# Performance work log

Measured on AMD Instinct MI355X. Metric: run time of the kernel, lower is better.

The kernel has to match this reference:

```python
import jax, jax.numpy as jnp
import numpy as np

B, H, W, C = 32, 56, 56, 128
WS, NH, DEPTH = 7, 4, 2
SHIFT = WS // 2
N = WS * WS
HID = 4 * C
CPB = 512


def _layernorm(x, g, b, eps=1e-5):
    m = x.mean(-1, keepdims=True)
    v = ((x - m) ** 2).mean(-1, keepdims=True)
    return (x - m) * jax.lax.rsqrt(v + eps) * g + b


def _window_partition(x):
    b, h, w, c = x.shape
    x = x.reshape(b, h // WS, WS, w // WS, WS, c)
    return x.transpose(0, 1, 3, 2, 4, 5).reshape(-1, N, c)


def _window_reverse(xw, h, w):
    c = xw.shape[-1]
    b = xw.shape[0] // ((h // WS) * (w // WS))
    x = xw.reshape(b, h // WS, w // WS, WS, WS, c)
    return x.transpose(0, 1, 3, 2, 4, 5).reshape(b, h, w, c)


def _rel_index():
    coords = np.stack(np.meshgrid(np.arange(WS), np.arange(WS), indexing='ij'))
    flat = coords.reshape(2, -1)
    rel = (flat[:, :, None] - flat[:, None, :]).transpose(1, 2, 0).astype(np.int64)
    rel[..., 0] += WS - 1
    rel[..., 1] += WS - 1
    rel[..., 0] *= 2 * WS - 1
    return jnp.asarray(rel.sum(-1))  # [N, N]


def _coords_table():
    # SwinV2 log-spaced continuous relative coords table (pretrained_window_size=0 path)
    r = np.arange(-(WS - 1), WS, dtype=np.float32)
    t = np.stack(np.meshgrid(r, r, indexing='ij'), axis=-1)  # [2W-1, 2W-1, 2]
    t = t / (WS - 1) * 8.0
    t = np.sign(t) * np.log2(np.abs(t) + 1.0) / np.log2(8.0)
    return jnp.asarray(t.reshape(-1, 2))  # [(2W-1)^2, 2]


def _shift_mask():
    img = np.zeros((H, W), np.float32)
    cnt = 0
    for hs in (slice(0, -WS), slice(-WS, -SHIFT), slice(-SHIFT, None)):
        for ws_ in (slice(0, -WS), slice(-WS, -SHIFT), slice(-SHIFT, None)):
            img[hs, ws_] = cnt
            cnt += 1
    mw = np.asarray(_window_partition(jnp.asarray(img)[None, :, :, None])).reshape(-1, N)
    diff = mw[:, None, :] - mw[:, :, None]
    return jnp.asarray(np.where(diff != 0, -100.0, 0.0).astype(np.float32))  # [nW, N, N]


def _forward(x, qkv_w, q_bias, v_bias, logit_scale, cpb_w1, cpb_b1, cpb_w2,
             proj_w, proj_b, norm1_g, norm1_b, mlp_w1, mlp_b1, mlp_w2, mlp_b2,
             norm2_g, norm2_b, pm_g, pm_b, pm_w):
    rel_idx = _rel_index()
    table = _coords_table()
    smask = _shift_mask()
    for i in range(DEPTH):
        shift = 0 if i % 2 == 0 else SHIFT
        xs = jnp.roll(x, (-shift, -shift), axis=(1, 2)) if shift else x
        xw = _window_partition(xs)  # [B*nW, N, C]
        bias = jnp.concatenate([q_bias[i], jnp.zeros_like(q_bias[i]), v_bias[i]])
        qkv = (xw @ qkv_w[i] + bias).reshape(-1, N, 3, NH, C // NH).transpose(2, 0, 3, 1, 4)
        q, k, v = qkv[0], qkv[1], qkv[2]  # [B*nW, NH, N, hd]
        qn = q / jnp.maximum(jnp.linalg.norm(q, axis=-1, keepdims=True), 1e-12)
        kn = k / jnp.maximum(jnp.linalg.norm(k, axis=-1, keepdims=True), 1e-12)
        scale = jnp.exp(jnp.minimum(logit_scale[i], jnp.log(100.0)))  # [NH,1,1]
        attn = jnp.einsum('bhnd,bhmd->bhnm', qn, kn) * scale
        rpb = 16.0 * jax.nn.sigmoid(
            (jax.nn.relu(table @ cpb_w1[i] + cpb_b1[i]) @ cpb_w2[i])[rel_idx])  # [N,N,NH]
        attn = attn + rpb.transpose(2, 0, 1)[None]
        if shift:
            nW = smask.shape[0]
            attn = (attn.reshape(-1, nW, NH, N, N) + smask[None, :, None]).reshape(-1, NH, N, N)
        attn = jax.nn.softmax(attn, axis=-1)
        out = jnp.einsum('bhnm,bhmd->bnhd', attn, v).reshape(-1, N, C)
        out = out @ proj_w[i] + proj_b[i]
        xs = _window_reverse(out, H, W)
        if shift:
            xs = jnp.roll(xs, (shift, shift), axis=(1, 2))
        # SwinV2 post-norm residuals
        x = x + _layernorm(xs, norm1_g[i], norm1_b[i])
        y = jax.nn.gelu(x @ mlp_w1[i] + mlp_b1[i], approximate=False) @ mlp_w2[i] + mlp_b2[i]
        x = x + _layernorm(y, norm2_g[i], norm2_b[i])
    # PatchMerging: [B,H,W,C] -> [B,H/2,W/2,4C] -> norm -> Linear(4C,2C)
    xm = x.reshape(B, H // 2, 2, W // 2, 2, C).transpose(0, 1, 3, 2, 4, 5)
    xm = xm.reshape(B, H // 2, W // 2, 4 * C)
    return _layernorm(xm, pm_g, pm_b) @ pm_w


def setup_inputs() -> dict:
    key = jax.random.key(0)
    ks = jax.random.split(key, 8)
    s = 0.02
    rn = lambda k, shp: jax.random.normal(k, shp, jnp.float32) * s
    return dict(
        x=jax.random.normal(ks[0], (B, H, W, C), jnp.float32),
        qkv_w=rn(ks[1], (DEPTH, C, 3 * C)),
        q_bias=jnp.zeros((DEPTH, C), jnp.float32),
        v_bias=jnp.zeros((DEPTH, C), jnp.float32),
        logit_scale=jnp.full((DEPTH, NH, 1, 1), np.log(10.0), jnp.float32),
        cpb_w1=rn(ks[2], (DEPTH, 2, CPB)),
        cpb_b1=jnp.zeros((DEPTH, CPB), jnp.float32),
        cpb_w2=rn(ks[3], (DEPTH, CPB, NH)),
        proj_w=rn(ks[4], (DEPTH, C, C)),
        proj_b=jnp.zeros((DEPTH, C), jnp.float32),
        norm1_g=jnp.ones((DEPTH, C), jnp.float32),
        norm1_b=jnp.zeros((DEPTH, C), jnp.float32),
        mlp_w1=rn(ks[5], (DEPTH, C, HID)),
        mlp_b1=jnp.zeros((DEPTH, HID), jnp.float32),
        mlp_w2=rn(ks[6], (DEPTH, HID, C)),
        mlp_b2=jnp.zeros((DEPTH, C), jnp.float32),
        norm2_g=jnp.ones((DEPTH, C), jnp.float32),
        norm2_b=jnp.zeros((DEPTH, C), jnp.float32),
        pm_g=jnp.ones((4 * C,), jnp.float32),
        pm_b=jnp.zeros((4 * C,), jnp.float32),
        pm_w=rn(ks[7], (4 * C, 2 * C)),
    )


def reference(x, qkv_w, q_bias, v_bias, logit_scale, cpb_w1, cpb_b1, cpb_w2,
              proj_w, proj_b, norm1_g, norm1_b, mlp_w1, mlp_b1, mlp_w2, mlp_b2,
              norm2_g, norm2_b, pm_g, pm_b, pm_w):
    return _forward(x, qkv_w, q_bias, v_bias, logit_scale, cpb_w1, cpb_b1, cpb_w2,
                    proj_w, proj_b, norm1_g, norm1_b, mlp_w1, mlp_b1, mlp_w2, mlp_b2,
                    norm2_g, norm2_b, pm_g, pm_b, pm_w)
```

## Files before the change

kernel.cpp:

```cpp
#include <hip/hip_runtime.h>
#include <math.h>


namespace {
constexpr int kTok = 32 * 56 * 56;
}

typedef __attribute__((ext_vector_type(8))) short bf16x8;
typedef __attribute__((ext_vector_type(4))) float f32x4;

union FragU {
    int4 i4;
    bf16x8 b8;
    unsigned short u[8];
};

__device__ __forceinline__ short f2bf(float f) {
    unsigned u = __float_as_uint(f);
    return (short)((u + 0x7FFFu + ((u >> 16) & 1u)) >> 16);
}
__device__ __forceinline__ float bf2f(unsigned short u) {
    return __uint_as_float(((unsigned)u) << 16);
}
__device__ __forceinline__ unsigned cvt_pk_bf16(float a, float b) {
    unsigned r;
    asm("v_cvt_pk_bf16_f32 %0, %1, %2" : "=v"(r) : "v"(a), "v"(b));
    return r;
}
__device__ __forceinline__ float gelu_t(float x) {
    float x2 = x * x;
    float t0 = fmaf(0.044715f * x2, x, x);
    float e = exp2f(2.3022227f * t0);
    float r = __builtin_amdgcn_rcpf(e + 1.0f);
    return fmaf(-x, r, x);
}

__global__ __launch_bounds__(256) void k_cpb(
    const float* __restrict__ w1, const float* __restrict__ b1,
    const float* __restrict__ w2, float* __restrict__ out169) {
    int L = blockIdx.x / 169;
    int t = blockIdx.x % 169;
    const float* w1L = w1 + L * 1024;
    const float* b1L = b1 + L * 512;
    const float* w2L = w2 + L * 2048;
    float* outL = out169 + L * 704;
    int ia = t / 13, ib = t % 13;
    float r0 = (float)(ia - 6) * (8.0f / 6.0f);
    float s0 = (r0 > 0.f) ? 1.f : (r0 < 0.f ? -1.f : 0.f);
    float t0 = s0 * log2f(fabsf(r0) + 1.0f) * (1.0f / 3.0f);
    float r1 = (float)(ib - 6) * (8.0f / 6.0f);
    float s1 = (r1 > 0.f) ? 1.f : (r1 < 0.f ? -1.f : 0.f);
    float t1 = s1 * log2f(fabsf(r1) + 1.0f) * (1.0f / 3.0f);

    int tid = threadIdx.x;
    float p0 = 0, p1 = 0, p2 = 0, p3 = 0;
    for (int c = tid; c < 512; c += 256) {
        float hv = fmaxf(t0 * w1L[c] + t1 * w1L[512 + c] + b1L[c], 0.0f);
        p0 += hv * w2L[c * 4 + 0];
        p1 += hv * w2L[c * 4 + 1];
        p2 += hv * w2L[c * 4 + 2];
        p3 += hv * w2L[c * 4 + 3];
    }
    __shared__ float red[256][4];
    red[tid][0] = p0; red[tid][1] = p1; red[tid][2] = p2; red[tid][3] = p3;
    __syncthreads();
    for (int s = 128; s > 0; s >>= 1) {
        if (tid < s) {
            red[tid][0] += red[tid + s][0];
            red[tid][1] += red[tid + s][1];
            red[tid][2] += red[tid + s][2];
            red[tid][3] += red[tid + s][3];
        }
        __syncthreads();
    }
    if (tid < 4) outL[t * 4 + tid] = red[0][tid];
}

__global__ void k_rpb(const float* __restrict__ out169, float* __restrict__ rpb64) {
    int e2 = blockIdx.x * 256 + threadIdx.x;
    int L = e2 >> 14, e = e2 & 16383;
    int h = e >> 12, r = e & 4095;
    int i = r >> 6, j = r & 63;
    float val;
    if (j >= 49) {
        val = -30000.0f;
    } else if (i >= 49) {
        val = 0.0f;
    } else {
        int dp = i / 7 - j / 7 + 6;
        int dq = i % 7 - j % 7 + 6;
        float v = out169[L * 704 + (dp * 13 + dq) * 4 + h];
        val = 16.0f / (1.0f + expf(-v));
    }
    rpb64[e2] = val;
}

__device__ __forceinline__ void cvt_slot(
    const float* __restrict__ W, short* __restrict__ Wb, int slt, int Kb, int N) {
    int nn = slt & 63;
    int tmp = slt >> 6;
    int kb = tmp % Kb;
    int nt = tmp / Kb;
    int n = nt * 64 + nn;
    int k0 = kb * 8;
    union { int4 i4; short s8[8]; } u;
#pragma unroll
    for (int e = 0; e < 8; ++e) u.s8[e] = f2bf(W[(size_t)(k0 + e) * N + n]);
    int nns = (nn & ~3) | ((nn ^ kb) & 3);
    *(int4*)(Wb + (((size_t)tmp) * 64 + nns) * 8) = u.i4;
}

__global__ __launch_bounds__(256) void k_cvtall(
    const float* __restrict__ qkv_w, const float* __restrict__ proj_w,
    const float* __restrict__ mw1, const float* __restrict__ mw2,
    const float* __restrict__ pmw, const float* __restrict__ qb,
    const float* __restrict__ vb, short* __restrict__ wall,
    float* __restrict__ bias384) {
    int s = blockIdx.x * 256 + threadIdx.x;
    short* wqkvb  = wall;
    short* wprojb = wall + 98304;
    short* wm1b   = wall + 131072;
    short* wm2b   = wall + 262144;
    short* wpmb   = wall + 393216;
    if (s < 12288) {
        int L = s / 6144, r = s % 6144;
        cvt_slot(qkv_w + L * 49152, wqkvb + L * 49152, r, 16, 384);
    } else if (s < 16384) {
        int s2 = s - 12288;
        int L = s2 / 2048, r = s2 % 2048;
        cvt_slot(proj_w + L * 16384, wprojb + L * 16384, r, 16, 128);
    } else if (s < 32768) {
        int s2 = s - 16384;
        int L = s2 / 8192, r = s2 % 8192;
        cvt_slot(mw1 + L * 65536, wm1b + L * 65536, r, 16, 512);
    } else if (s < 49152) {
        int s2 = s - 32768;
        int L = s2 / 8192, r = s2 % 8192;
        cvt_slot(mw2 + L * 65536, wm2b + L * 65536, r, 64, 128);
    } else if (s < 65536) {
        cvt_slot(pmw, wpmb, s - 49152, 64, 256);
    } else if (s < 66304) {
        int t = s - 65536;
        int L = t / 384, f = t % 384;
        float v = (f < 128) ? qb[L * 128 + f]
                            : ((f < 256) ? 0.0f : vb[L * 128 + f - 256]);
        bias384[t] = v;
    }
}

__global__ __launch_bounds__(256) void k_cvtx(
    const float* __restrict__ x, short* __restrict__ xb) {
    size_t e = ((size_t)blockIdx.x * 256 + threadIdx.x) * 8;
    const float* src = x + e;
    float4 f0 = *(const float4*)src;
    float4 f1 = *(const float4*)(src + 4);
    union { int4 i4; short s8[8]; } u;
    u.s8[0] = f2bf(f0.x); u.s8[1] = f2bf(f0.y);
    u.s8[2] = f2bf(f0.z); u.s8[3] = f2bf(f0.w);
    u.s8[4] = f2bf(f1.x); u.s8[5] = f2bf(f1.y);
    u.s8[6] = f2bf(f1.z); u.s8[7] = f2bf(f1.w);
    *(int4*)(xb + e) = u.i4;
}

template <int K, int NT>
__global__ __launch_bounds__(256) void k_gemm(
    const short* __restrict__ Ain, const short* __restrict__ Wb,
    float* __restrict__ Out, int ostride) {
    constexpr int Kb = K / 8;
    constexpr int NC = K / 128;
    __shared__ int4 As4[2048];
    __shared__ int4 Ws4[1024];
    int tid = threadIdx.x;
    int nwg = gridDim.x;
    int chunk = nwg >> 3;
    int lid = (blockIdx.x & 7) * chunk + (blockIdx.x >> 3);
    int mt = lid / NT, nt = lid - mt * NT;
    int mb = mt * 128;
    int w = tid >> 6, l = tid & 63, lr = l & 15, lg = l >> 4;
    const f32x4 fz = {0.f, 0.f, 0.f, 0.f};
    f32x4 acc[2][4];
#pragma unroll
    for (int mi = 0; mi < 2; ++mi)
#pragma unroll
        for (int ni = 0; ni < 4; ++ni) acc[mi][ni] = fz;

    for (int c = 0; c < NC; ++c) {
        if (c) __syncthreads();
#pragma unroll
        for (int it = 0; it < 8; ++it) {
            int s = it * 256 + tid;
            int m = s >> 4, kb = s & 15;
            int slot = kb * 128 + ((m & ~7) | ((m ^ kb) & 7));
            As4[slot] = *(const int4*)(Ain + (size_t)(mb + m) * K + c * 128 + kb * 8);
        }
        {
            const int4* wsrc = (const int4*)(Wb + ((size_t)nt * Kb + c * 16) * 64 * 8);
#pragma unroll
            for (int it = 0; it < 4; ++it) Ws4[it * 256 + tid] = wsrc[it * 256 + tid];
        }
        __syncthreads();
#pragma unroll
        for (int kk = 0; kk < 4; ++kk) {
            int kbl = kk * 4 + lg;
            int m0 = w * 32 + lr;
            bf16x8 a0 = *(const bf16x8*)&As4[kbl * 128 + ((m0 & ~7) | ((m0 ^ kbl) & 7))];
            int m1 = m0 + 16;
            bf16x8 a1 = *(const bf16x8*)&As4[kbl * 128 + ((m1 & ~7) | ((m1 ^ kbl) & 7))];
#pragma unroll
            for (int ni = 0; ni < 4; ++ni) {
                int nn = lr + 16 * ni;
                bf16x8 bfr = *(const bf16x8*)&Ws4[kbl * 64 + ((nn & ~3) | ((nn ^ kbl) & 3))];
                acc[0][ni] = __builtin_amdgcn_mfma_f32_16x16x32_bf16(a0, bfr, acc[0][ni], 0, 0, 0);
                acc[1][ni] = __builtin_amdgcn_mfma_f32_16x16x32_bf16(a1, bfr, acc[1][ni], 0, 0, 0);
            }
        }
    }
#pragma unroll
    for (int ni = 0; ni < 4; ++ni) {
        int col = nt * 64 + ni * 16 + lr;
#pragma unroll
        for (int mi = 0; mi < 2; ++mi) {
#pragma unroll
            for (int r = 0; r < 4; ++r) {
                int row = mb + w * 32 + mi * 16 + lg * 4 + r;
                Out[(size_t)row * ostride + col] = acc[mi][ni][r];
            }
        }
    }
}

template <int K, bool RF32>
__global__ __launch_bounds__(256) void k_gemm_ln(
    const short* __restrict__ Ain, const short* __restrict__ Wb,
    const float* __restrict__ bias, const float* __restrict__ g,
    const float* __restrict__ bt, const void* __restrict__ resid,
    short* __restrict__ xoutb, int shift) {
    constexpr int Kb = K / 8;
    constexpr int NC = K / 128;
    __shared__ int4 As4[1024];
    __shared__ int4 Ws4[2048];
    int tid = threadIdx.x;
    int mb = blockIdx.x * 64;
    int w = tid >> 6, l = tid & 63, lr = l & 15, lg = l >> 4;
    const f32x4 fz = {0.f, 0.f, 0.f, 0.f};
    f32x4 acc[8];
#pragma unroll
    for (int ni = 0; ni < 8; ++ni) acc[ni] = fz;

    for (int c = 0; c < NC; ++c) {
        if (c) __syncthreads();
#pragma unroll
        for (int it = 0; it < 4; ++it) {
            int s = it * 256 + tid;
            int m = s >> 4, kb = s & 15;
            int slot = kb * 64 + ((m & ~7) | ((m ^ kb) & 7));
            As4[slot] = *(const int4*)(Ain + (size_t)(mb + m) * K + c * 128 + kb * 8);
        }
        {
            const int4* w0 = (const int4*)(Wb + ((size_t)(c * 16)) * 64 * 8);
            const int4* w1 = (const int4*)(Wb + ((size_t)(Kb + c * 16)) * 64 * 8);
#pragma unroll
            for (int it = 0; it < 4; ++it) {
                Ws4[it * 256 + tid] = w0[it * 256 + tid];
                Ws4[1024 + it * 256 + tid] = w1[it * 256 + tid];
            }
        }
        __syncthreads();
#pragma unroll
        for (int kk = 0; kk < 4; ++kk) {
            int kbl = kk * 4 + lg;
            int m0 = w * 16 + lr;
            bf16x8 a0 = *(const bf16x8*)&As4[kbl * 64 + ((m0 & ~7) | ((m0 ^ kbl) & 7))];
#pragma unroll
            for (int ni = 0; ni < 8; ++ni) {
                int nn = lr + 16 * (ni & 3);
                bf16x8 bfr = *(const bf16x8*)&Ws4[(ni >> 2) * 1024 + kbl * 64 +
                                                  ((nn & ~3) | ((nn ^ kbl) & 3))];
                acc[ni] = __builtin_amdgcn_mfma_f32_16x16x32_bf16(a0, bfr, acc[ni], 0, 0, 0);
            }
        }
    }
    float bv[8], gv[8], btv[8];
#pragma unroll
    for (int ni = 0; ni < 8; ++ni) {
        int col = ni * 16 + lr;
        bv[ni] = bias[col]; gv[ni] = g[col]; btv[ni] = bt[col];
    }
#pragma unroll
    for (int r = 0; r < 4; ++r) {
        int row = mb + w * 16 + lg * 4 + r;
        float v[8];
        float s1 = 0.f, s2 = 0.f;
#pragma unroll
        for (int ni = 0; ni < 8; ++ni) {
            v[ni] = acc[ni][r] + bv[ni];
            s1 += v[ni];
            s2 = fmaf(v[ni], v[ni], s2);
        }
#pragma unroll
        for (int off = 8; off >= 1; off >>= 1) {
            s1 += __shfl_xor(s1, off);
            s2 += __shfl_xor(s2, off);
        }
        float mean = s1 * (1.0f / 128.0f);
        float var = s2 * (1.0f / 128.0f) - mean * mean;
        float rstd = rsqrtf(var + 1e-5f);
        int mo = row;
        if (shift) {
            int b = row / 3136, rr = row % 3136;
            int hh = rr / 56 + shift; if (hh >= 56) hh -= 56;
            int ww = rr % 56 + shift; if (ww >= 56) ww -= 56;
            mo = b * 3136 + hh * 56 + ww;
        }
        size_t base = (size_t)mo * 128;
#pragma unroll
        for (int ni = 0; ni < 8; ++ni) {
            int col = ni * 16 + lr;
            float rv = RF32 ? ((const float*)resid)[base + col]
                            : bf2f(((const unsigned short*)resid)[base + col]);
            float o = rv + (v[ni] - mean) * rstd * gv[ni] + btv[ni];
            xoutb[base + col] = f2bf(o);
        }
    }
}

__global__ __launch_bounds__(256) void k_mlp(
    short* __restrict__ xb, const short* __restrict__ W1b,
    const short* __restrict__ W2b, const float* __restrict__ b1,
    const float* __restrict__ b2, const float* __restrict__ g,
    const float* __restrict__ bt) {
    __shared__ int4 W1s[1024];
    __shared__ int4 W2s[1024];
    __shared__ short Hs[4 * 2304];
    int tid = threadIdx.x;
    int mb = blockIdx.x * 128;
    int w = tid >> 6, l = tid & 63, lr = l & 15, lg = l >> 4;
    const f32x4 fz = {0.f, 0.f, 0.f, 0.f};
    short* Hw = Hs + w * 2304;

    int4 xfrag[2][4];
#pragma unroll
    for (int mi = 0; mi < 2; ++mi)
#pragma unroll
        for (int kk = 0; kk < 4; ++kk)
            xfrag[mi][kk] = *(const int4*)(
                xb + (size_t)(mb + w * 32 + mi * 16 + lr) * 128 + kk * 32 + lg * 8);

    f32x4 acc2[2][8];
#pragma unroll
    for (int mi = 0; mi < 2; ++mi)
#pragma unroll
        for (int ni = 0; ni < 8; ++ni) acc2[mi][ni] = fz;

    for (int c = 0; c < 8; ++c) {
        __syncthreads();
        {
            const int4* w1src = (const int4*)(W1b + (size_t)c * 8192);
#pragma unroll
            for (int it = 0; it < 4; ++it) W1s[it * 256 + tid] = w1src[it * 256 + tid];
            const int4* w2a = (const int4*)(W2b + (size_t)(c * 8) * 512);
            const int4* w2c = (const int4*)(W2b + (size_t)(64 + c * 8) * 512);
#pragma unroll
            for (int it = 0; it < 2; ++it) {
                W2s[it * 256 + tid] = w2a[it * 256 + tid];
                W2s[512 + it * 256 + tid] = w2c[it * 256 + tid];
            }
        }
        __syncthreads();
        f32x4 a1[2][4];
#pragma unroll
        for (int mi = 0; mi < 2; ++mi)
#pragma unroll
            for (int ct = 0; ct < 4; ++ct) a1[mi][ct] = fz;
        __builtin_amdgcn_s_setprio(1);
#pragma unroll
        for (int kk = 0; kk < 4; ++kk) {
            int kbl = kk * 4 + lg;
            FragU xa0; xa0.i4 = xfrag[0][kk];
            FragU xa1; xa1.i4 = xfrag[1][kk];
#pragma unroll
            for (int ct = 0; ct < 4; ++ct) {
                int nn = lr + 16 * ct;
                bf16x8 w1f = *(const bf16x8*)&W1s[kbl * 64 + ((nn & ~3) | ((nn ^ kbl) & 3))];
                a1[0][ct] = __builtin_amdgcn_mfma_f32_16x16x32_bf16(w1f, xa0.b8, a1[0][ct], 0, 0, 0);
                a1[1][ct] = __builtin_amdgcn_mfma_f32_16x16x32_bf16(w1f, xa1.b8, a1[1][ct], 0, 0, 0);
            }
        }
        __builtin_amdgcn_s_setprio(0);
#pragma unroll
        for (int mi = 0; mi < 2; ++mi) {
#pragma unroll
            for (int ct = 0; ct < 4; ++ct) {
                float4 bb = *(const float4*)(b1 + c * 64 + ct * 16 + lg * 4);
                float h0 = gelu_t(a1[mi][ct][0] + bb.x);
                float h1 = gelu_t(a1[mi][ct][1] + bb.y);
                float h2 = gelu_t(a1[mi][ct][2] + bb.z);
                float h3 = gelu_t(a1[mi][ct][3] + bb.w);
                unsigned p0 = cvt_pk_bf16(h0, h1);
                unsigned p1 = cvt_pk_bf16(h2, h3);
                *(int2*)&Hw[(mi * 16 + lr) * 72 + ct * 16 + lg * 4] =
                    make_int2((int)p0, (int)p1);
            }
        }
        __builtin_amdgcn_s_setprio(1);
#pragma unroll
        for (int kc = 0; kc < 2; ++kc) {
            int kbl = kc * 4 + lg;
            FragU ha0; ha0.i4 = *(const int4*)&Hw[lr * 72 + kc * 32 + lg * 8];
            FragU ha1; ha1.i4 = *(const int4*)&Hw[(16 + lr) * 72 + kc * 32 + lg * 8];
#pragma unroll
            for (int ni = 0; ni < 8; ++ni) {
                int nn = lr + 16 * (ni & 3);
                bf16x8 w2f = *(const bf16x8*)&W2s[(ni >> 2) * 512 + kbl * 64 +
                                                  ((nn & ~3) | ((nn ^ kbl) & 3))];
                acc2[0][ni] = __builtin_amdgcn_mfma_f32_16x16x32_bf16(ha0.b8, w2f, acc2[0][ni], 0, 0, 0);
                acc2[1][ni] = __builtin_amdgcn_mfma_f32_16x16x32_bf16(ha1.b8, w2f, acc2[1][ni], 0, 0, 0);
            }
        }
        __builtin_amdgcn_s_setprio(0);
    }

    float bv[8], gv[8], btv[8];
#pragma unroll
    for (int ni = 0; ni < 8; ++ni) {
        int col = ni * 16 + lr;
        bv[ni] = b2[col]; gv[ni] = g[col]; btv[ni] = bt[col];
    }
#pragma unroll
    for (int mi = 0; mi < 2; ++mi) {
#pragma unroll
        for (int r = 0; r < 4; ++r) {
            int row = mb + w * 32 + mi * 16 + lg * 4 + r;
            float v[8];
            float s1 = 0.f, s2 = 0.f;
#pragma unroll
            for (int ni = 0; ni < 8; ++ni) {
                v[ni] = acc2[mi][ni][r] + bv[ni];
                s1 += v[ni];
                s2 = fmaf(v[ni], v[ni], s2);
            }
#pragma unroll
            for (int off = 8; off >= 1; off >>= 1) {
                s1 += __shfl_xor(s1, off);
                s2 += __shfl_xor(s2, off);
            }
            float mean = s1 * (1.0f / 128.0f);
            float var = s2 * (1.0f / 128.0f) - mean * mean;
            float rstd = rsqrtf(var + 1e-5f);
            size_t base = (size_t)row * 128;
#pragma unroll
            for (int ni = 0; ni < 8; ++ni) {
                int col = ni * 16 + lr;
                float rv = bf2f(((const unsigned short*)xb)[base + col]);
                float o = rv + (v[ni] - mean) * rstd * gv[ni] + btv[ni];
                xb[base + col] = f2bf(o);
            }
        }
    }
}

__global__ __launch_bounds__(256) void k_attn(
    const short* __restrict__ xb, const short* __restrict__ Wq,
    const float* __restrict__ bias384, const float* __restrict__ rpb64,
    const float* __restrict__ ls, short* __restrict__ aout, int shift) {
    __shared__ short qkvs[64 * 392];
    __shared__ short pvt[4 * 3584];
    int wid = blockIdx.x;
    int b = wid >> 6, wrem = wid & 63;
    int wh = wrem >> 3, ww_ = wrem & 7;
    int tid = threadIdx.x;
    int w = tid >> 6;
    int l = tid & 63, lr = l & 15, lg = l >> 4;
    int tokbase = b * 3136 + wh * 7 * 56 + ww_ * 7;
    const f32x4 fz = {0.f, 0.f, 0.f, 0.f};

    {
        int ti = w * 16 + lr;
        bool valid = (ti < 49);
        int4 xfrag[4];
        const int4 zero4 = make_int4(0, 0, 0, 0);
        if (valid) {
            int m = tokbase + (ti / 7) * 56 + (ti % 7);
            if (shift) {
                int bb2 = m / 3136, rr = m % 3136;
                int hh = rr / 56 + shift; if (hh >= 56) hh -= 56;
                int ww2 = rr % 56 + shift; if (ww2 >= 56) ww2 -= 56;
                m = bb2 * 3136 + hh * 56 + ww2;
            }
#pragma unroll
            for (int kk = 0; kk < 4; ++kk)
                xfrag[kk] = *(const int4*)(xb + (size_t)m * 128 + kk * 32 + lg * 8);
        } else {
#pragma unroll
            for (int kk = 0; kk < 4; ++kk) xfrag[kk] = zero4;
        }
        short* orow = qkvs + (w * 16 + lr) * 392;
#pragma unroll
        for (int ft = 0; ft < 24; ++ft) {
            f32x4 a = fz;
            int n = ft * 16 + lr;
            int nt = n >> 6, nn = n & 63;
#pragma unroll
            for (int kk = 0; kk < 4; ++kk) {
                int kbl = kk * 4 + lg;
                int nns = (nn & ~3) | ((nn ^ kbl) & 3);
                bf16x8 wf = *(const bf16x8*)(Wq + (((size_t)nt * 16 + kbl) * 64 + nns) * 8);
                FragU xa; xa.i4 = xfrag[kk];
                a = __builtin_amdgcn_mfma_f32_16x16x32_bf16(wf, xa.b8, a, 0, 0, 0);
            }
            float4 bb = *(const float4*)(bias384 + ft * 16 + lg * 4);
            unsigned p0 = cvt_pk_bf16(a[0] + bb.x, a[1] + bb.y);
            unsigned p1 = cvt_pk_bf16(a[2] + bb.z, a[3] + bb.w);
            *(int2*)&orow[ft * 16 + lg * 4] = make_int2((int)p0, (int)p1);
        }
    }
    __syncthreads();

    int h = w;
    short* Pt = pvt + h * 3584;
    short* Vt = Pt + 1152;
    float* invks = (float*)(Vt + 2304);

    float scale = __expf(fminf(ls[h], 4.6051702f));
    int4 qf[4], kf[4];
#pragma unroll
    for (int t = 0; t < 4; ++t) {
        const short* base = qkvs + (t * 16 + lr) * 392 + h * 32 + lg * 8;
        qf[t] = *(const int4*)base;
        kf[t] = *(const int4*)(base + 128);
    }

    float invq[4];
#pragma unroll
    for (int t = 0; t < 4; ++t) {
        {
            FragU u; u.i4 = qf[t];
            float ss = 0.f;
#pragma unroll
            for (int e = 0; e < 8; ++e) { float x = bf2f(u.u[e]); ss = fmaf(x, x, ss); }
            ss += __shfl_xor(ss, 16);
            ss += __shfl_xor(ss, 32);
            invq[t] = scale / fmaxf(sqrtf(ss), 1e-12f);
        }
        {
            FragU u; u.i4 = kf[t];
            float ss = 0.f;
#pragma unroll
            for (int e = 0; e < 8; ++e) { float x = bf2f(u.u[e]); ss = fmaf(x, x, ss); }
            ss += __shfl_xor(ss, 16);
            ss += __shfl_xor(ss, 32);
            float ik = 1.0f / fmaxf(sqrtf(ss), 1e-12f);
            if (l < 16) invks[t * 16 + l] = ik;
        }
    }

    for (int t = l; t < 480; t += 64) {
        Vt[(t / 15) * 72 + 49 + (t % 15)] = 0;
    }
#pragma unroll
    for (int t = 0; t < 4; ++t) {
        int e = t * 64 + l;
        int j = e >> 2, dq = e & 3;
        if (j < 49) {
            FragU u;
            u.i4 = *(const int4*)(qkvs + j * 392 + 256 + h * 32 + dq * 8);
#pragma unroll
            for (int ee = 0; ee < 8; ++ee) Vt[(dq * 8 + ee) * 72 + j] = (short)u.u[ee];
        }
    }

    float ika[4][4];
#pragma unroll
    for (int jt = 0; jt < 4; ++jt) {
        float4 v4 = *(const float4*)&invks[jt * 16 + lg * 4];
        ika[jt][0] = v4.x; ika[jt][1] = v4.y; ika[jt][2] = v4.z; ika[jt][3] = v4.w;
    }

    bool edge = (shift != 0) && ((wh == 7) || (ww_ == 7));
    const float* rbase = rpb64 + h * 4096;
    f32x4 oacc[2][4];
#pragma unroll
    for (int mi = 0; mi < 2; ++mi)
#pragma unroll
        for (int ni = 0; ni < 4; ++ni) oacc[mi][ni] = fz;

#pragma unroll
    for (int qt = 0; qt < 4; ++qt) {
        f32x4 at[4];
        __builtin_amdgcn_s_setprio(1);
#pragma unroll
        for (int jt = 0; jt < 4; ++jt) {
            FragU a; a.i4 = kf[jt];
            FragU bq; bq.i4 = qf[qt];
            at[jt] = __builtin_amdgcn_mfma_f32_16x16x32_bf16(a.b8, bq.b8, fz, 0, 0, 0);
        }
        __builtin_amdgcn_s_setprio(0);

        float iq = invq[qt];
        int qi = qt * 16 + lr;
        int qc = (qi < 49) ? qi : 48;
        int rlq = 0, clq = 0;
        if (edge) {
            rlq = (wh == 7) ? ((qc / 7) < 4 ? 1 : 2) : 0;
            clq = (ww_ == 7) ? ((qc % 7) < 4 ? 1 : 2) : 0;
        }
#pragma unroll
        for (int jt = 0; jt < 4; ++jt) {
            float4 rv = *(const float4*)(rbase + qc * 64 + jt * 16 + lg * 4);
            float rr[4] = {rv.x, rv.y, rv.z, rv.w};
#pragma unroll
            for (int r = 0; r < 4; ++r) {
                float v = fmaf(at[jt][r] * ika[jt][r], iq, rr[r]);
                if (edge) {
                    int j = jt * 16 + lg * 4 + r;
                    int jc = (j < 49) ? j : 48;
                    int rlk = (wh == 7) ? ((jc / 7) < 4 ? 1 : 2) : 0;
                    int clk = (ww_ == 7) ? ((jc % 7) < 4 ? 1 : 2) : 0;
                    if (rlk != rlq || clk != clq) v -= 100.0f;
                }
                at[jt][r] = v;
            }
        }
        float m = -1e30f;
#pragma unroll
        for (int jt = 0; jt < 4; ++jt)
#pragma unroll
            for (int r = 0; r < 4; ++r) m = fmaxf(m, at[jt][r]);
        m = fmaxf(m, __shfl_xor(m, 16));
        m = fmaxf(m, __shfl_xor(m, 32));
        float s = 0.f;
#pragma unroll
        for (int jt = 0; jt < 4; ++jt)
#pragma unroll
            for (int r = 0; r < 4; ++r) {
                float p = __expf(at[jt][r] - m);
                at[jt][r] = p;
                s += p;
            }
        s += __shfl_xor(s, 16);
        s += __shfl_xor(s, 32);
        float inv = 1.0f / s;
#pragma unroll
        for (int jt = 0; jt < 4; ++jt) {
            unsigned lo = cvt_pk_bf16(at[jt][0] * inv, at[jt][1] * inv);
            unsigned hi = cvt_pk_bf16(at[jt][2] * inv, at[jt][3] * inv);
            *(int2*)&Pt[lr * 72 + jt * 16 + lg * 4] = make_int2((int)lo, (int)hi);
        }
        __builtin_amdgcn_s_setprio(1);
#pragma unroll
        for (int kc = 0; kc < 2; ++kc) {
            FragU pb;
            pb.i4 = *(const int4*)&Pt[lr * 72 + kc * 32 + lg * 8];
#pragma unroll
            for (int mi = 0; mi < 2; ++mi) {
                FragU va;
                va.i4 = *(const int4*)&Vt[(mi * 16 + lr) * 72 + kc * 32 + lg * 8];
                oacc[mi][qt] = __builtin_amdgcn_mfma_f32_16x16x32_bf16(
                    va.b8, pb.b8, oacc[mi][qt], 0, 0, 0);
            }
        }
        __builtin_amdgcn_s_setprio(0);
    }

#pragma unroll
    for (int ni = 0; ni < 4; ++ni) {
        int qrow = ni * 16 + lr;
        if (qrow < 49) {
            int tok = tokbase + (qrow / 7) * 56 + (qrow % 7);
#pragma unroll
            for (int mi = 0; mi < 2; ++mi) {
                unsigned lo = cvt_pk_bf16(oacc[mi][ni][0], oacc[mi][ni][1]);
                unsigned hi = cvt_pk_bf16(oacc[mi][ni][2], oacc[mi][ni][3]);
                *(int2*)&aout[(size_t)tok * 128 + h * 32 + mi * 16 + lg * 4] =
                    make_int2((int)lo, (int)hi);
            }
        }
    }
}

__global__ __launch_bounds__(256) void k_pmln(
    const short* __restrict__ x, const float* __restrict__ g,
    const float* __restrict__ bt, short* __restrict__ outb) {
    int m2 = blockIdx.x * 4 + (threadIdx.x >> 6);
    int l = threadIdx.x & 63;
    int b = m2 / 784, r = m2 % 784;
    int h2 = r / 28, w2 = r % 28;
    int q0 = l * 8;
    int i2 = q0 >> 8, j2 = (q0 >> 7) & 1, c = q0 & 127;
    const short* src = x + (size_t)((b * 56 + 2 * h2 + i2) * 56 + 2 * w2 + j2) * 128 + c;
    FragU u; u.i4 = *(const int4*)src;
    float v[8];
#pragma unroll
    for (int e = 0; e < 8; ++e) v[e] = bf2f(u.u[e]);
    float s1 = 0.f, s2 = 0.f;
#pragma unroll
    for (int e = 0; e < 8; ++e) { s1 += v[e]; s2 = fmaf(v[e], v[e], s2); }
#pragma unroll
    for (int off = 32; off >= 1; off >>= 1) {
        s1 += __shfl_xor(s1, off);
        s2 += __shfl_xor(s2, off);
    }
    float mean = s1 * (1.0f / 512.0f);
    float var = s2 * (1.0f / 512.0f) - mean * mean;
    float rstd = rsqrtf(var + 1e-5f);
    union { int4 i4; short s8[8]; } o;
#pragma unroll
    for (int e = 0; e < 8; ++e)
        o.s8[e] = f2bf((v[e] - mean) * rstd * g[q0 + e] + bt[q0 + e]);
    *(int4*)(outb + (size_t)m2 * 512 + q0) = o.i4;
}

extern "C" void kernel_launch(void* const* d_in, const int* in_sizes, int n_in,
                              void* d_out, int out_size, void* d_ws, size_t ws_size,
                              hipStream_t stream) {
    const float* x_in   = (const float*)d_in[0];
    const float* qkv_w  = (const float*)d_in[1];
    const float* q_bias = (const float*)d_in[2];
    const float* v_bias = (const float*)d_in[3];
    const float* lscale = (const float*)d_in[4];
    const float* cpb_w1 = (const float*)d_in[5];
    const float* cpb_b1 = (const float*)d_in[6];
    const float* cpb_w2 = (const float*)d_in[7];
    const float* proj_w = (const float*)d_in[8];
    const float* proj_b = (const float*)d_in[9];
    const float* n1g    = (const float*)d_in[10];
    const float* n1b    = (const float*)d_in[11];
    const float* mw1    = (const float*)d_in[12];
    const float* mb1    = (const float*)d_in[13];
    const float* mw2    = (const float*)d_in[14];
    const float* mb2    = (const float*)d_in[15];
    const float* n2g    = (const float*)d_in[16];
    const float* n2b    = (const float*)d_in[17];
    const float* pmg    = (const float*)d_in[18];
    const float* pmb    = (const float*)d_in[19];
    const float* pmw    = (const float*)d_in[20];
    float* out = (float*)d_out;

    float* wsf    = (float*)d_ws;
    short* wall   = (short*)wsf;
    short* wqkvb  = wall;
    short* wprojb = wall + 98304;
    short* wm1b   = wall + 131072;
    short* wm2b   = wall + 262144;
    short* wpmb   = wall + 393216;
    float* out169 = wsf + 262144;
    float* rpb64  = out169 + 1408;
    float* bias384 = rpb64 + 32768;

    float* R1      = wsf + (size_t)12845056;
    short* attnout = (short*)(R1 + (size_t)19267584);
    short* pmin    = (short*)R1;
    short* xb      = (short*)(R1 + (size_t)25690112);

    k_cvtall<<<260, 256, 0, stream>>>(qkv_w, proj_w, mw1, mw2, pmw,
                                      q_bias, v_bias, wall, bias384);
    k_cpb<<<338, 256, 0, stream>>>(cpb_w1, cpb_b1, cpb_w2, out169);
    k_rpb<<<128, 256, 0, stream>>>(out169, rpb64);
    k_cvtx<<<6272, 256, 0, stream>>>(x_in, xb);

    for (int i = 0; i < 2; ++i) {
        int shift = i ? 3 : 0;
        k_attn<<<2048, 256, 0, stream>>>(
            xb, wqkvb + i * 49152, bias384 + i * 384, rpb64 + i * 16384,
            lscale + i * 4, attnout, shift);
        if (i == 0) {
            k_gemm_ln<128, true><<<1568, 256, 0, stream>>>(
                attnout, wprojb, proj_b, n1g, n1b, x_in, xb, shift);
        } else {
            k_gemm_ln<128, false><<<1568, 256, 0, stream>>>(
                attnout, wprojb + 16384, proj_b + 128, n1g + 128, n1b + 128,
                xb, xb, shift);
        }
        k_mlp<<<784, 256, 0, stream>>>(
            xb, wm1b + i * 65536, wm2b + i * 65536, mb1 + i * 512,
            mb2 + i * 128, n2g + i * 128, n2b + i * 128);
    }
    k_pmln<<<6272, 256, 0, stream>>>(xb, pmg, pmb, pmin);
    k_gemm<512, 4><<<784, 256, 0, stream>>>(pmin, wpmb, out, 256);
}
```

Before: 354.8 us.

## Write V transposed directly from QKV MFMA and shrink attention LDS footprint

The QKV projection now stores V straight into a per-head transposed LDS buffer instead of writing it row-major and transposing it in a later pass. The qkv staging buffer drops to Q and K only, and the P scratch reuses that buffer after an extra barrier. The inverse key norms are passed between lanes with shuffles instead of going through LDS. Together these cut LDS traffic and total LDS per block, which may allow more blocks per CU. The costs are an added __syncthreads and scattered 2-byte transposed stores; the zero padding of V columns 49..63 is no longer written explicitly.

```diff
diff --git a/kernel.cpp b/kernel.cpp
--- a/kernel.cpp
+++ b/kernel.cpp
@@ -463,8 +463,8 @@
     const short* __restrict__ xb, const short* __restrict__ Wq,
     const float* __restrict__ bias384, const float* __restrict__ rpb64,
     const float* __restrict__ ls, short* __restrict__ aout, int shift) {
-    __shared__ short qkvs[64 * 392];
-    __shared__ short pvt[4 * 3584];
+    __shared__ short qkvs[64 * 264];
+    __shared__ short Vth[4 * 2304];
     int wid = blockIdx.x;
     int b = wid >> 6, wrem = wid & 63;
     int wh = wrem >> 3, ww_ = wrem & 7;
@@ -494,7 +494,7 @@
 #pragma unroll
             for (int kk = 0; kk < 4; ++kk) xfrag[kk] = zero4;
         }
-        short* orow = qkvs + (w * 16 + lr) * 392;
+        short* orow = qkvs + (w * 16 + lr) * 264;
 #pragma unroll
         for (int ft = 0; ft < 24; ++ft) {
             f32x4 a = fz;
@@ -509,28 +509,39 @@
                 a = __builtin_amdgcn_mfma_f32_16x16x32_bf16(wf, xa.b8, a, 0, 0, 0);
             }
             float4 bb = *(const float4*)(bias384 + ft * 16 + lg * 4);
-            unsigned p0 = cvt_pk_bf16(a[0] + bb.x, a[1] + bb.y);
-            unsigned p1 = cvt_pk_bf16(a[2] + bb.z, a[3] + bb.w);
-            *(int2*)&orow[ft * 16 + lg * 4] = make_int2((int)p0, (int)p1);
+            if (ft < 16) {
+                unsigned p0 = cvt_pk_bf16(a[0] + bb.x, a[1] + bb.y);
+                unsigned p1 = cvt_pk_bf16(a[2] + bb.z, a[3] + bb.w);
+                *(int2*)&orow[ft * 16 + lg * 4] = make_int2((int)p0, (int)p1);
+            } else {
+                int f = ft - 16;
+                int h2 = f >> 1;
+                int dbase = (f & 1) * 16 + lg * 4;
+                int tok = w * 16 + lr;
+                short* vdst = Vth + h2 * 2304 + dbase * 72 + tok;
+                float av[4] = {a[0] + bb.x, a[1] + bb.y, a[2] + bb.z, a[3] + bb.w};
+#pragma unroll
+                for (int r = 0; r < 4; ++r) vdst[r * 72] = f2bf(av[r]);
+            }
         }
     }
     __syncthreads();
 
     int h = w;
-    short* Pt = pvt + h * 3584;
-    short* Vt = Pt + 1152;
-    float* invks = (float*)(Vt + 2304);
+    short* Vt = Vth + h * 2304;
 
     float scale = __expf(fminf(ls[h], 4.6051702f));
     int4 qf[4], kf[4];
 #pragma unroll
     for (int t = 0; t < 4; ++t) {
-        const short* base = qkvs + (t * 16 + lr) * 392 + h * 32 + lg * 8;
+        const short* base = qkvs + (t * 16 + lr) * 264 + h * 32 + lg * 8;
         qf[t] = *(const int4*)base;
         kf[t] = *(const int4*)(base + 128);
     }
-
-    float invq[4];
+    __syncthreads();
+    short* Pt = qkvs + h * 1152;
+
+    float invq[4], ikreg[4];
 #pragma unroll
     for (int t = 0; t < 4; ++t) {
         {
@@ -549,32 +560,15 @@
             for (int e = 0; e < 8; ++e) { float x = bf2f(u.u[e]); ss = fmaf(x, x, ss); }
             ss += __shfl_xor(ss, 16);
             ss += __shfl_xor(ss, 32);
-            float ik = 1.0f / fmaxf(sqrtf(ss), 1e-12f);
-            if (l < 16) invks[t * 16 + l] = ik;
-        }
-    }
-
-    for (int t = l; t < 480; t += 64) {
-        Vt[(t / 15) * 72 + 49 + (t % 15)] = 0;
-    }
-#pragma unroll
-    for (int t = 0; t < 4; ++t) {
-        int e = t * 64 + l;
-        int j = e >> 2, dq = e & 3;
-        if (j < 49) {
-            FragU u;
-            u.i4 = *(const int4*)(qkvs + j * 392 + 256 + h * 32 + dq * 8);
-#pragma unroll
-            for (int ee = 0; ee < 8; ++ee) Vt[(dq * 8 + ee) * 72 + j] = (short)u.u[ee];
-        }
-    }
-
+            ikreg[t] = 1.0f / fmaxf(sqrtf(ss), 1e-12f);
+        }
+    }
     float ika[4][4];
 #pragma unroll
-    for (int jt = 0; jt < 4; ++jt) {
-        float4 v4 = *(const float4*)&invks[jt * 16 + lg * 4];
-        ika[jt][0] = v4.x; ika[jt][1] = v4.y; ika[jt][2] = v4.z; ika[jt][3] = v4.w;
-    }
+    for (int jt = 0; jt < 4; ++jt)
+#pragma unroll
+        for (int r = 0; r < 4; ++r)
+            ika[jt][r] = __shfl(ikreg[jt], lg * 4 + r);
 
     bool edge = (shift != 0) && ((wh == 7) || (ww_ == 7));
     const float* rbase = rpb64 + h * 4096;
```

Result: faster. 336.0 us (-5.3%).
